# Performance work log

Hardware: AMD Instinct MI355X
Metric: run time of the kernel (lower is better)

The kernel has to match this reference:

```python
import jax, jax.numpy as jnp
import numpy as np

T, D = 4096, 2048
H, DK, DV = 6, 256, 512        # heads, head_k_dim, head_v_dim (expand_v=2)
KD, VD = H * DK, H * DV        # 1536, 3072
KSZ = 4                        # conv_size
GEN = D // 8                   # generator reduction 8 -> 256
EPS = 1e-5                     # norm_eps


def setup_inputs() -> dict:
    key = jax.random.key(0)
    ks = jax.random.split(key, 12)
    std = 0.02
    p = lambda i, shape: jax.random.normal(ks[i], shape, jnp.float32) * std
    rng = np.random.default_rng(0)
    A = rng.uniform(0.0, 16.0, H).astype(np.float32)
    dt = np.exp(rng.uniform(0, 1, H) * (np.log(0.1) - np.log(0.001)) + np.log(0.001)).astype(np.float32)
    dt = np.clip(dt, 1e-4, None)
    inv_dt = (dt + np.log(-np.expm1(-dt))).astype(np.float32)
    return {
        'hidden_states': jax.random.normal(ks[0], (T, D), jnp.float32),
        'Wq': p(1, (D, KD)), 'Wk': p(2, (D, KD)), 'Wv': p(3, (D, VD)),
        'Wb': p(4, (D, H)), 'Wa': p(5, (D, H)), 'Wg': p(6, (D, VD)), 'Wo': p(7, (VD, D)),
        'A_log': jnp.asarray(np.log(A)), 'dt_bias': jnp.asarray(inv_dt),
        'conv_w': p(8, (VD, KSZ)), 'gen_w1': p(9, (D, GEN)), 'gen_w2': p(10, (GEN, KSZ)),
        'norm_w': jnp.ones((DV,), jnp.float32),
    }


def _l2norm(x):
    return x * jax.lax.rsqrt(jnp.sum(x * x, -1, keepdims=True) + 1e-6)


def reference(hidden_states, Wq, Wk, Wv, Wb, Wa, Wg, Wo, A_log, dt_bias, conv_w, gen_w1, gen_w2, norm_w):
    h = hidden_states[None]                             # [1,T,D]
    q = jax.nn.silu(h @ Wq)                             # [1,T,KD]
    k = jax.nn.silu(h @ Wk)
    x = h @ Wv                                          # [1,T,VD]
    # dynamic short convolution: per-token kernel added to static depthwise kernel
    dyn = jax.nn.silu(h @ gen_w1) @ gen_w2              # [1,T,KSZ]
    xpad = jnp.pad(x, ((0, 0), (KSZ - 1, 0), (0, 0)))   # causal padding
    v = jnp.zeros_like(x)
    for j in range(KSZ):
        v = v + (conv_w[None, None, :, j] + dyn[:, :, None, j]) * xpad[:, j:j + x.shape[1], :]
    v = jax.nn.silu(v)

    B = 1
    q = _l2norm(q.reshape(B, -1, H, DK))                # use_qk_l2norm_in_kernel=True
    k = _l2norm(k.reshape(B, -1, H, DK))
    v = v.reshape(B, -1, H, DV)
    beta = jax.nn.sigmoid(h @ Wb)                       # [1,T,H]
    g = -jnp.exp(A_log) * jax.nn.softplus(h @ Wa + dt_bias)  # [1,T,H] decay log-gates
    scale = DK ** -0.5

    def step(S, inp):                                   # gated delta rule recurrence
        qt, kt, vt, gt, bt = inp
        S = S * jnp.exp(gt)[..., None, None]            # [B,H,DK,DV]
        dv = (vt - jnp.einsum('bhk,bhkv->bhv', kt, S)) * bt[..., None]
        S = S + kt[..., :, None] * dv[..., None, :]
        ot = jnp.einsum('bhk,bhkv->bhv', qt, S) * scale
        return S, ot

    S0 = jnp.zeros((B, H, DK, DV), jnp.float32)
    tm = lambda a: jnp.moveaxis(a, 1, 0)                # time-major for scan
    _, o = jax.lax.scan(step, S0, (tm(q), tm(k), tm(v), tm(g), tm(beta)))
    o = jnp.moveaxis(o, 0, 1)                           # [1,T,H,DV]

    gate = (h @ Wg).reshape(B, -1, H, DV)
    rms = jax.lax.rsqrt(jnp.mean(o * o, -1, keepdims=True) + EPS)
    o = o * rms * norm_w * jax.nn.silu(gate)            # gated RMSNorm
    o = o.reshape(B, -1, VD) @ Wo                       # [1,T,D]
    return o[0]
```

## Files before the change

### kernel.cpp

```cpp
#include <hip/hip_runtime.h>
#include <hip/hip_bf16.h>
#include <math.h>

#define T_LEN 4096
#define DIM   2048
#define NH    6
#define DK    256
#define DVh   512
#define KD    1536
#define VD    3072
#define CK    64
#define NCHK  (T_LEN / CK)

typedef __attribute__((ext_vector_type(8))) short bf16x8;
typedef __attribute__((ext_vector_type(4))) float f32x4;

__device__ __forceinline__ float silu_f(float v){ return v / (1.f + __expf(-v)); }

__device__ __forceinline__ unsigned short f2bf(float f) {
  unsigned int u = __float_as_uint(f);
  unsigned int r = u + 0x7FFFu + ((u >> 16) & 1u);
  return (unsigned short)(r >> 16);
}
__device__ __forceinline__ float bf2f(unsigned short s) {
  return __uint_as_float(((unsigned int)s) << 16);
}

__device__ __forceinline__ void bar_lds() {
  __builtin_amdgcn_sched_barrier(0);
  asm volatile("s_waitcnt lgkmcnt(0)" ::: "memory");
  __builtin_amdgcn_s_barrier();
  __builtin_amdgcn_sched_barrier(0);
}

__global__ __launch_bounds__(256) void cast_bf16(
    const float* __restrict__ in, unsigned short* __restrict__ out)
{
  int i = blockIdx.x * 256 + threadIdx.x;
  float4 v4 = ((const float4*)in)[i];
  ushort4 o4;
  o4.x = f2bf(v4.x); o4.y = f2bf(v4.y); o4.z = f2bf(v4.z); o4.w = f2bf(v4.w);
  ((ushort4*)out)[i] = o4;
}

__global__ __launch_bounds__(256) void tcast(
// ... 58 lines not shown
#pragma unroll
    for (int i = 0; i < 4; ++i)
#pragma unroll
      for (int j = 0; j < 4; ++j)
        acc[i][j] = __builtin_amdgcn_mfma_f32_16x16x32_bf16(af[i], bfr[j], acc[i][j], 0, 0, 0);
    __syncthreads();
  }

  if (act == 2) {
    unsigned short* C = (unsigned short*)Cout;
#pragma unroll
    for (int i = 0; i < 4; ++i) {
      int rbase = bm + wm + i * 16 + kq * 4;
#pragma unroll
      for (int r = 0; r < 4; ++r) {
        size_t rowoff = (size_t)(rbase + r) * N + bn + wn + fr;
#pragma unroll
        for (int j = 0; j < 4; ++j) C[rowoff + j * 16] = f2bf(acc[i][j][r]);
      }
    }
  } else {
    float* C = (float*)Cout;
#pragma unroll
    for (int i = 0; i < 4; ++i) {
      int rbase = bm + wm + i * 16 + kq * 4;
#pragma unroll
      for (int r = 0; r < 4; ++r) {
        size_t rowoff = (size_t)(rbase + r) * N + bn + wn + fr;
#pragma unroll
        for (int j = 0; j < 4; ++j) {
          float v = acc[i][j][r];
          if (act == 1) v = silu_f(v);
          C[rowoff + j * 16] = v;
        }
      }
    }
  }
}

__global__ __launch_bounds__(256) void proj_dyn(
    const float* __restrict__ tg, const float* __restrict__ w2, float* __restrict__ dyn)
{
  int t = blockIdx.x, tid = threadIdx.x;
  float g = tg[(size_t)t * 256 + tid];
  float p[4];
#pragma unroll
  for (int j = 0; j < 4; ++j) p[j] = g * w2[tid * 4 + j];
#pragma unroll
  for (int j = 0; j < 4; ++j)
    for (int m = 32; m >= 1; m >>= 1) p[j] += __shfl_xor(p[j], m);
  __shared__ float red[4][4];
  if ((tid & 63) == 0) {
    int w = tid >> 6;
#pragma unroll
    for (int j = 0; j < 4; ++j) red[w][j] = p[j];
  }
  __syncthreads();
  if (tid < 4) dyn[(size_t)t * 4 + tid] = red[0][tid] + red[1][tid] + red[2][tid] + red[3][tid];
}

__global__ __launch_bounds__(256) void proj_bg(
    const float* __restrict__ h, const float* __restrict__ Wb, const float* __restrict__ Wa,
    const float* __restrict__ A_log, const float* __restrict__ dt_bias,
    float* __restrict__ beta, float* __restrict__ gout)
{
  int t = blockIdx.x, tid = threadIdx.x;
// ... 14 lines not shown
  __shared__ float rb[4][6], ra[4][6];
  if ((tid & 63) == 0) {
    int w = tid >> 6;
#pragma unroll
    for (int j = 0; j < 6; ++j) { rb[w][j] = pb[j]; ra[w][j] = pa[j]; }
  }
  __syncthreads();
  if (tid < 6) {
    int j = tid;
    float sb = rb[0][j] + rb[1][j] + rb[2][j] + rb[3][j];
    float sa = ra[0][j] + ra[1][j] + ra[2][j] + ra[3][j];
    beta[(size_t)t * 6 + j] = 1.f / (1.f + expf(-sb));
    float z = sa + dt_bias[j];
    float sp = (z > 20.f) ? z : log1pf(expf(z));
    gout[(size_t)t * 6 + j] = -expf(A_log[j]) * sp;
  }
}

__global__ __launch_bounds__(256) void conv_kernel(
    const float* __restrict__ x, const float* __restrict__ dyn,
    const float* __restrict__ cw, float* __restrict__ v)
{
  int c = blockIdx.x * 256 + threadIdx.x;
  int t = blockIdx.y;
  float4 w4 = ((const float4*)cw)[c];
  float d0 = dyn[t * 4 + 0], d1 = dyn[t * 4 + 1], d2 = dyn[t * 4 + 2], d3 = dyn[t * 4 + 3];
  float acc = (w4.w + d3) * x[(size_t)t * VD + c];
  if (t >= 1) acc += (w4.z + d2) * x[(size_t)(t - 1) * VD + c];
  if (t >= 2) acc += (w4.y + d1) * x[(size_t)(t - 2) * VD + c];
  if (t >= 3) acc += (w4.x + d0) * x[(size_t)(t - 3) * VD + c];
  v[(size_t)t * VD + c] = silu_f(acc);
}

__global__ __launch_bounds__(64) void l2norm_qk(
    float* __restrict__ q, float* __restrict__ k)
{
  size_t base = (size_t)blockIdx.x * 256;
  int tid = threadIdx.x;
  float4 qv = ((float4*)(q + base))[tid];
  float4 kv = ((float4*)(k + base))[tid];
  float sq = qv.x*qv.x + qv.y*qv.y + qv.z*qv.z + qv.w*qv.w;
  float sk = kv.x*kv.x + kv.y*kv.y + kv.z*kv.z + kv.w*kv.w;
  for (int m = 32; m >= 1; m >>= 1) { sq += __shfl_xor(sq, m); sk += __shfl_xor(sk, m); }
  float rq = rsqrtf(sq + 1e-6f) * 0.0625f;
  float rk = rsqrtf(sk + 1e-6f);
  qv.x *= rq; qv.y *= rq; qv.z *= rq; qv.w *= rq;
  kv.x *= rk; kv.y *= rk; kv.z *= rk; kv.w *= rk;
  ((float4*)(q + base))[tid] = qv;
  ((float4*)(k + base))[tid] = kv;
}

__global__ __launch_bounds__(64) void cumsum_g(
    const float* __restrict__ g, float* __restrict__ c, float* __restrict__ gammas)
{
  int ch = blockIdx.x, h = blockIdx.y;
  int t0 = ch * CK;
  int lane = threadIdx.x;
  float cum = g[(size_t)(t0 + lane) * 6 + h];
  for (int off = 1; off < 64; off <<= 1) {
    float n = __shfl_up(cum, off);
    if (lane >= off) cum += n;
  }
  c[(size_t)h * T_LEN + t0 + lane] = cum;
  if (lane == 63) gammas[h * NCHK + ch] = __expf(cum);
}

__global__ __launch_bounds__(384) void scale_kq(
    const float* __restrict__ q, const float* __restrict__ k, const float* __restrict__ c,
    unsigned short* __restrict__ Qb, unsigned short* __restrict__ Kb)
{
  int t = blockIdx.x;
  int tid = threadIdx.x;
  int h = tid >> 6;
  float w1 = __expf(c[(size_t)h * T_LEN + t]);
  size_t off = (size_t)t * KD + tid * 4;
  float4 qv = *(const float4*)(q + off);
  float4 kv = *(const float4*)(k + off);
  ushort4 qo, ko;
  qo.x = f2bf(w1 * qv.x); qo.y = f2bf(w1 * qv.y); qo.z = f2bf(w1 * qv.z); qo.w = f2bf(w1 * qv.w);
  ko.x = f2bf(w1 * kv.x); ko.y = f2bf(w1 * kv.y); ko.z = f2bf(w1 * kv.z); ko.w = f2bf(w1 * kv.w);
  *(ushort4*)(Qb + off) = qo;
  *(ushort4*)(Kb + off) = ko;
}

__global__ __launch_bounds__(256) void make_khT(
    const float* __restrict__ k, const float* __restrict__ c,
    unsigned short* __restrict__ KhT)
{
  int ch = blockIdx.x, h = blockIdx.y;
  int t0 = ch * CK;
  int tt = threadIdx.x & 63, ks = threadIdx.x >> 6;
  float cend = c[(size_t)h * T_LEN + t0 + 63];
  float w2 = __expf(cend - c[(size_t)h * T_LEN + t0 + tt]);
  size_t obase = ((size_t)(h * NCHK + ch)) * DK * CK;
#pragma unroll 8
  for (int kb2 = 0; kb2 < 64; ++kb2) {
    int kk = ks * 64 + kb2;
    float kv = k[(size_t)(t0 + tt) * KD + h * 256 + kk];
    KhT[obase + (size_t)kk * CK + tt] = f2bf(w2 * kv);
  }
}

__global__ __launch_bounds__(256) void chunk_lp(
    const float* __restrict__ q, const float* __restrict__ k,
    const float* __restrict__ c, const float* __restrict__ beta,
    float* __restrict__ Lg, unsigned short* __restrict__ Pm)
{
  const int ch = blockIdx.x, h = blockIdx.y;
  const int t0 = ch * CK;
  const int tid = threadIdx.x;
// ... 16 lines not shown
  if (tid < 64) {
    cs[tid] = c[(size_t)h * T_LEN + t0 + tid];
    bs[tid] = beta[(size_t)(t0 + tid) * 6 + h];
  }
  __syncthreads();

  f32x4 akk[4], aqk[4];
#pragma unroll
  for (int j = 0; j < 4; ++j) { akk[j] = (f32x4){0,0,0,0}; aqk[j] = (f32x4){0,0,0,0}; }
#pragma unroll
  for (int kt = 0; kt < 8; ++kt) {
    bf16x8 ak = *(const bf16x8*)&kb[16 * w + fr][kt * 32 + kq * 8];
    bf16x8 aq = *(const bf16x8*)&qb[16 * w + fr][kt * 32 + kq * 8];
#pragma unroll
    for (int j = 0; j < 4; ++j) {
      bf16x8 b = *(const bf16x8*)&kb[j * 16 + fr][kt * 32 + kq * 8];
      akk[j] = __builtin_amdgcn_mfma_f32_16x16x32_bf16(ak, b, akk[j], 0, 0, 0);
      aqk[j] = __builtin_amdgcn_mfma_f32_16x16x32_bf16(aq, b, aqk[j], 0, 0, 0);
    }
  }
  size_t base = ((size_t)(h * NCHK + ch)) * CK * CK;
#pragma unroll
  for (int j = 0; j < 4; ++j) {
#pragma unroll
    for (int r = 0; r < 4; ++r) {
      int t = 16 * w + kq * 4 + r, col = j * 16 + fr;
      float e = __expf(fminf(cs[t] - cs[col], 0.f));
      Lg[base + t * 64 + col] = (col < t) ? bs[t] * e * akk[j][r] : 0.f;
      Pm[base + t * 64 + col] = f2bf((col <= t) ? e * aqk[j][r] : 0.f);
    }
  }
}

__global__ __launch_bounds__(64) void tri_inv(
    const float* __restrict__ Lg, const float* __restrict__ beta,
    unsigned short* __restrict__ Tm)
{
  const int ch = blockIdx.x, h = blockIdx.y;
  const size_t base = ((size_t)(h * NCHK + ch)) * CK * CK;
  const int j = threadIdx.x;
  __shared__ float Ll[64][65];
  __shared__ float Tl[64][65];
  for (int t = 0; t < 64; ++t) Ll[t][j] = Lg[base + t * 64 + j];
  __syncthreads();
  for (int t = 0; t < 64; ++t) {
    float s;
    if (j > t) s = 0.f;
    else if (j == t) s = 1.f;
    else {
      s = 0.f;
      for (int m = j; m < t; ++m) s -= Ll[t][m] * Tl[m][j];
    }
    Tl[t][j] = s;
  }
  float bj = beta[(size_t)(ch * 64 + j) * 6 + h];
  for (int t = 0; t < 64; ++t) Tm[base + t * 64 + j] = f2bf(Tl[t][j] * bj);
}

__global__ __launch_bounds__(512, 2) void scan_chunk(
    const unsigned short* __restrict__ Kb,
    const unsigned short* __restrict__ Qb,
    const unsigned short* __restrict__ KhT,
    const unsigned short* __restrict__ Tm,
    const unsigned short* __restrict__ Pm,
    const float* __restrict__ gammas,
    float* __restrict__ VO)
{
  const int h = blockIdx.y, sl = blockIdx.x;
  const int tid = threadIdx.x;
  const int w = tid >> 6, lane = tid & 63;
  const int tw = w & 3, kg = w >> 2;
  const int fr = lane & 15, kq = lane >> 4;

  __shared__ unsigned short S0h[16][264];
  __shared__ unsigned short S0l[16][264];
  __shared__ unsigned short XT[16][72];
  __shared__ unsigned short DVT[16][72];
  __shared__ float PY[2][4][16][20];
  __shared__ float PO[2][4][16][20];

  f32x4 st[2];
  st[0] = (f32x4){0.f, 0.f, 0.f, 0.f};
  st[1] = (f32x4){0.f, 0.f, 0.f, 0.f};

  const int colg = h * DVh + sl * 16 + fr;
  const size_t hc0 = (size_t)h * NCHK;

  {
    int zr = tid >> 5;
    int zc = (tid & 31) * 8;
    ushort4 z; z.x = 0; z.y = 0; z.z = 0; z.w = 0;
    *(ushort4*)&S0h[zr][zc]     = z;
    *(ushort4*)&S0h[zr][zc + 4] = z;
    *(ushort4*)&S0l[zr][zc]     = z;
    *(ushort4*)&S0l[zr][zc + 4] = z;
  }

  bf16x8 kfA[4], kfB[4], qfA[4], qfB[4];
  float vlA[4], vlB[4];

#define PREF(KF, QF, VL, chn) do { \
    const unsigned short* kr_ = Kb + (size_t)((chn) * CK + 16 * tw + fr) * KD + h * 256 + kg * 128 + kq * 8; \
    const unsigned short* qr_ = Qb + (size_t)((chn) * CK + 16 * tw + fr) * KD + h * 256 + kg * 128 + kq * 8; \
    _Pragma("unroll") \
    for (int kt = 0; kt < 4; ++kt) { \
      KF[kt] = *(const bf16x8*)(kr_ + kt * 32); \
      QF[kt] = *(const bf16x8*)(qr_ + kt * 32); } \
    if (kg == 0) { \
      _Pragma("unroll") \
      for (int r = 0; r < 4; ++r) VL[r] = VO[(size_t)((chn) * CK + 16 * tw + kq * 4 + r) * VD + colg]; } \
  } while (0)

#define BODY(chx, KF, QF, VL, KFN, QFN, VLN) do { \
    const int ch_ = (chx); \
    const int t0_ = ch_ * CK; \
    const size_t cb_ = hc0 + ch_; \
     \
    bf16x8 tpf[2]; \
    { const unsigned short* b_ = (kg == 0 ? Tm : Pm) + (cb_ * CK + 16 * tw + fr) * CK + kq * 8; \
      tpf[0] = *(const bf16x8*)(b_); tpf[1] = *(const bf16x8*)(b_ + 32); } \
    bf16x8 hfr[2][2]; \
    _Pragma("unroll") \
    for (int i = 0; i < 2; ++i) { \
      const unsigned short* hr_ = KhT + (cb_ * DK + 32 * w + 16 * i + fr) * CK + kq * 8; \
      hfr[i][0] = *(const bf16x8*)(hr_); hfr[i][1] = *(const bf16x8*)(hr_ + 32); } \
    const float gam_ = gammas[cb_]; \
    { const int chn_ = (ch_ + 1 < NCHK) ? ch_ + 1 : ch_; PREF(KFN, QFN, VLN, chn_); } \
     \
    f32x4 yt, ot; \
    { f32x4 yh = (f32x4){0.f,0.f,0.f,0.f}, yl = yh, oh = yh, ol = yh; \
      __builtin_amdgcn_s_setprio(1); \
      _Pragma("unroll") \
      for (int kt = 0; kt < 4; ++kt) { \
        const int ka_ = (kg * 4 + kt) * 32 + kq * 8; \
        bf16x8 bh_ = *(const bf16x8*)&S0h[fr][ka_]; \
        bf16x8 bl_ = *(const bf16x8*)&S0l[fr][ka_]; \
        yh = __builtin_amdgcn_mfma_f32_16x16x32_bf16(KF[kt], bh_, yh, 0, 0, 0); \
        yl = __builtin_amdgcn_mfma_f32_16x16x32_bf16(KF[kt], bl_, yl, 0, 0, 0); \
        oh = __builtin_amdgcn_mfma_f32_16x16x32_bf16(QF[kt], bh_, oh, 0, 0, 0); \
        ol = __builtin_amdgcn_mfma_f32_16x16x32_bf16(QF[kt], bl_, ol, 0, 0, 0); } \
      __builtin_amdgcn_s_setprio(0); \
      yt = yh + yl; ot = oh + ol; } \
    *(f32x4*)&PY[kg][tw][fr][kq * 4] = yt; \
    *(f32x4*)&PO[kg][tw][fr][kq * 4] = ot; \
    bar_lds();    \
    if (kg == 0) { \
      f32x4 yo = *(const f32x4*)&PY[1][tw][fr][kq * 4]; \
      ushort4 x4; \
      x4.x = f2bf(VL[0] - (yt[0] + yo[0])); \
      x4.y = f2bf(VL[1] - (yt[1] + yo[1])); \
      x4.z = f2bf(VL[2] - (yt[2] + yo[2])); \
      x4.w = f2bf(VL[3] - (yt[3] + yo[3])); \
      *(ushort4*)&XT[fr][16 * tw + kq * 4] = x4; \
    } else { \
      f32x4 oo = *(const f32x4*)&PO[0][tw][fr][kq * 4]; \
      ot[0] += oo[0]; ot[1] += oo[1]; ot[2] += oo[2]; ot[3] += oo[3]; } \
    bar_lds();    \
     \
    if (kg == 0) { \
      f32x4 d = (f32x4){0.f,0.f,0.f,0.f}; \
      bf16x8 b0_ = *(const bf16x8*)&XT[fr][kq * 8]; \
      bf16x8 b1_ = *(const bf16x8*)&XT[fr][32 + kq * 8]; \
      d = __builtin_amdgcn_mfma_f32_16x16x32_bf16(tpf[0], b0_, d, 0, 0, 0); \
      d = __builtin_amdgcn_mfma_f32_16x16x32_bf16(tpf[1], b1_, d, 0, 0, 0); \
      ushort4 d4; \
      d4.x = f2bf(d[0]); d4.y = f2bf(d[1]); d4.z = f2bf(d[2]); d4.w = f2bf(d[3]); \
      *(ushort4*)&DVT[fr][16 * tw + kq * 4] = d4; } \
    bar_lds();    \
     \
    { bf16x8 dv0_ = *(const bf16x8*)&DVT[fr][kq * 8]; \
      bf16x8 dv1_ = *(const bf16x8*)&DVT[fr][32 + kq * 8]; \
      if (kg == 1) { \
        f32x4 op = (f32x4){0.f,0.f,0.f,0.f}; \
        op = __builtin_amdgcn_mfma_f32_16x16x32_bf16(tpf[0], dv0_, op, 0, 0, 0); \
        op = __builtin_amdgcn_mfma_f32_16x16x32_bf16(tpf[1], dv1_, op, 0, 0, 0); \
        _Pragma("unroll") \
        for (int r = 0; r < 4; ++r) \
          VO[(size_t)(t0_ + 16 * tw + kq * 4 + r) * VD + colg] = ot[r] + op[r]; } \
      __builtin_amdgcn_s_setprio(1); \
      _Pragma("unroll") \
      for (int i = 0; i < 2; ++i) { \
        st[i][0] *= gam_; st[i][1] *= gam_; st[i][2] *= gam_; st[i][3] *= gam_; \
        st[i] = __builtin_amdgcn_mfma_f32_16x16x32_bf16(hfr[i][0], dv0_, st[i], 0, 0, 0); \
        st[i] = __builtin_amdgcn_mfma_f32_16x16x32_bf16(hfr[i][1], dv1_, st[i], 0, 0, 0); \
        ushort4 hi4, lo4; \
        { float s0 = st[i][0], s1 = st[i][1], s2 = st[i][2], s3 = st[i][3]; \
          hi4.x = f2bf(s0); lo4.x = f2bf(s0 - bf2f(hi4.x)); \
          hi4.y = f2bf(s1); lo4.y = f2bf(s1 - bf2f(hi4.y)); \
          hi4.z = f2bf(s2); lo4.z = f2bf(s2 - bf2f(hi4.z)); \
          hi4.w = f2bf(s3); lo4.w = f2bf(s3 - bf2f(hi4.w)); } \
        *(ushort4*)&S0h[fr][32 * w + 16 * i + kq * 4] = hi4; \
        *(ushort4*)&S0l[fr][32 * w + 16 * i + kq * 4] = lo4; } \
      __builtin_amdgcn_s_setprio(0); } \
    bar_lds();    \
  } while (0)

  PREF(kfA, qfA, vlA, 0);
  __syncthreads();
  for (int ch = 0; ch < NCHK; ch += 2) {
    BODY(ch,     kfA, qfA, vlA, kfB, qfB, vlB);
    BODY(ch + 1, kfB, qfB, vlB, kfA, qfA, vlA);
  }
#undef BODY
#undef PREF
}

__global__ __launch_bounds__(256) void norm_gate(
    const float* __restrict__ o, const unsigned short* __restrict__ gate,
    const float* __restrict__ nw, unsigned short* __restrict__ out)
{
  int th = blockIdx.x, tid = threadIdx.x;
  size_t base = (size_t)th * DVh;
  float x0 = o[base + tid], x1 = o[base + 256 + tid];
  float ss = x0 * x0 + x1 * x1;
  for (int m = 32; m >= 1; m >>= 1) ss += __shfl_xor(ss, m);
  __shared__ float red[4];
  if ((tid & 63) == 0) red[tid >> 6] = ss;
  __syncthreads();
  float rms = rsqrtf((red[0] + red[1] + red[2] + red[3]) * (1.f / 512.f) + 1e-5f);
  float g0 = bf2f(gate[base + tid]), g1 = bf2f(gate[base + 256 + tid]);
  out[base + tid]       = f2bf(x0 * rms * nw[tid]       * silu_f(g0));
  out[base + 256 + tid] = f2bf(x1 * rms * nw[tid + 256] * silu_f(g1));
}

extern "C" void kernel_launch(void* const* d_in, const int* in_sizes, int n_in,
                              void* d_out, int out_size, void* d_ws, size_t ws_size,
                              hipStream_t stream)
{
  const float* h       = (const float*)d_in[0];
  const float* Wq      = (const float*)d_in[1];
  const float* Wk      = (const float*)d_in[2];
  const float* Wv      = (const float*)d_in[3];
  const float* Wb      = (const float*)d_in[4];
  const float* Wa      = (const float*)d_in[5];
  const float* Wg      = (const float*)d_in[6];
  const float* Wo      = (const float*)d_in[7];
  const float* A_log   = (const float*)d_in[8];
  const float* dt_bias = (const float*)d_in[9];
  const float* conv_w  = (const float*)d_in[10];
  const float* gen_w1  = (const float*)d_in[11];
  const float* gen_w2  = (const float*)d_in[12];
  const float* norm_w  = (const float*)d_in[13];
  float* out = (float*)d_out;

  const size_t TK = (size_t)T_LEN * KD, TV = (size_t)T_LEN * VD, TD = (size_t)T_LEN * DIM;

  float* ws   = (float*)d_ws;
  float* q    = ws;
  float* k    = q    + TK;
  float* x    = k    + TK;
  float* v    = x    + TV;
  float* tg   = v    + TV;
  float* dyn  = tg   + (size_t)T_LEN * 256;
  float* beta = dyn  + (size_t)T_LEN * 4;
  float* g    = beta + (size_t)T_LEN * 6;
  float* c    = g    + (size_t)T_LEN * 6;
  float* gam  = c    + (size_t)NH * T_LEN;
  float* fend = gam  + 512;
  unsigned short* bh      = (unsigned short*)fend;
  unsigned short* wT      = bh      + TD;
  unsigned short* gate_bf = wT      + (size_t)DIM * VD;
  unsigned short* go_bf   = gate_bf + TV;
  unsigned short* Kb_s  = bh;
  unsigned short* Qb_s  = (unsigned short*)x;
  unsigned short* KhT_s = Qb_s + TK;
  unsigned short* Tm_s  = KhT_s + TK;
  unsigned short* Pm_s  = Tm_s + (size_t)NH * NCHK * CK * CK;
  float* Lg = (float*)go_bf;

  dim3 blk(256);
  cast_bf16<<<(TD / 4) / 256, blk, 0, stream>>>(h, bh);
  tcast<<<dim3(KD / 32, DIM / 32), blk, 0, stream>>>(Wq, wT, DIM, KD);
  gemm_bt_bf16<<<dim3(KD / 128, T_LEN / 128), blk, 0, stream>>>(bh, wT, q, T_LEN, KD, DIM, 1);
  tcast<<<dim3(KD / 32, DIM / 32), blk, 0, stream>>>(Wk, wT, DIM, KD);
  gemm_bt_bf16<<<dim3(KD / 128, T_LEN / 128), blk, 0, stream>>>(bh, wT, k, T_LEN, KD, DIM, 1);
  tcast<<<dim3(VD / 32, DIM / 32), blk, 0, stream>>>(Wv, wT, DIM, VD);
  gemm_bt_bf16<<<dim3(VD / 128, T_LEN / 128), blk, 0, stream>>>(bh, wT, x, T_LEN, VD, DIM, 0);
  tcast<<<dim3(VD / 32, DIM / 32), blk, 0, stream>>>(Wg, wT, DIM, VD);
  gemm_bt_bf16<<<dim3(VD / 128, T_LEN / 128), blk, 0, stream>>>(bh, wT, gate_bf, T_LEN, VD, DIM, 2);
  tcast<<<dim3(256 / 32, DIM / 32), blk, 0, stream>>>(gen_w1, wT, DIM, 256);
  gemm_bt_bf16<<<dim3(256 / 128, T_LEN / 128), blk, 0, stream>>>(bh, wT, tg, T_LEN, 256, DIM, 1);

  proj_dyn<<<T_LEN, blk, 0, stream>>>(tg, gen_w2, dyn);
  proj_bg<<<T_LEN, blk, 0, stream>>>(h, Wb, Wa, A_log, dt_bias, beta, g);
  conv_kernel<<<dim3(VD / 256, T_LEN), blk, 0, stream>>>(x, dyn, conv_w, v);
  l2norm_qk<<<T_LEN * NH, 64, 0, stream>>>(q, k);

  cumsum_g<<<dim3(NCHK, NH), 64, 0, stream>>>(g, c, gam);
  scale_kq<<<T_LEN, 384, 0, stream>>>(q, k, c, Qb_s, Kb_s);
  make_khT<<<dim3(NCHK, NH), blk, 0, stream>>>(k, c, KhT_s);
  chunk_lp<<<dim3(NCHK, NH), blk, 0, stream>>>(q, k, c, beta, Lg, Pm_s);
  tri_inv<<<dim3(NCHK, NH), 64, 0, stream>>>(Lg, beta, Tm_s);

  scan_chunk<<<dim3(DVh / 16, NH), 512, 0, stream>>>(Kb_s, Qb_s, KhT_s, Tm_s, Pm_s, gam, v);

  norm_gate<<<T_LEN * NH, blk, 0, stream>>>(v, gate_bf, norm_w, go_bf);
  tcast<<<dim3(DIM / 32, VD / 32), blk, 0, stream>>>(Wo, wT, VD, DIM);
  gemm_bt_bf16<<<dim3(DIM / 128, T_LEN / 128), blk, 0, stream>>>(go_bf, wT, out, T_LEN, DIM, VD, 0);
}
```

Measured before the change: 1.035 ms.

## Process chunk pairs in scan with precomputed cross-chunk interaction matrices

Adds a cross_lp kernel that precomputes, for each pair of consecutive chunks, the decayed K2·K1ᵀ and Q2·K1ᵀ interaction matrices. The sequential scan now advances two chunks per iteration. The second chunk's state projections reuse the first chunk's pre-update state, corrected through these matrices. This halves the number of serial state reads and LDS round-trips along the critical path, and removes the cross-warp partial-sum reduction. The cost is an extra kernel, more register pressure (launch bounds drop to one block per SM), and additional bf16 rounding in the correction terms.

```diff
diff --git a/kernel.cpp b/kernel.cpp
--- a/kernel.cpp
+++ b/kernel.cpp
@@ -11,6 +11,7 @@
 #define VD    3072
 #define CK    64
 #define NCHK  (T_LEN / CK)
+#define NPAIR (NCHK / 2)
 
 typedef __attribute__((ext_vector_type(8))) short bf16x8;
 typedef __attribute__((ext_vector_type(4))) float f32x4;
@@ -341,6 +342,63 @@
   }
 }
 
+__global__ __launch_bounds__(256) void cross_lp(
+    const unsigned short* __restrict__ Kb, const unsigned short* __restrict__ Qb,
+    const float* __restrict__ k, const float* __restrict__ c,
+    unsigned short* __restrict__ W21, unsigned short* __restrict__ U21)
+{
+  const int p = blockIdx.x, h = blockIdx.y;
+  const int t01 = p * 128, t02 = t01 + 64;
+  const int tid = threadIdx.x;
+  const int w = tid >> 6, lane = tid & 63, fr = lane & 15, kq = lane >> 4;
+  __shared__ float wg[64];
+  if (tid < 64) {
+    float cend = c[(size_t)h * T_LEN + t01 + 63];
+    wg[tid] = __expf(cend - c[(size_t)h * T_LEN + t01 + tid]);
+  }
+  __syncthreads();
+  bf16x8 kfr[8], qfr[8];
+  {
+    const unsigned short* kr = Kb + (size_t)(t02 + 16 * w + fr) * KD + h * 256 + kq * 8;
+    const unsigned short* qr = Qb + (size_t)(t02 + 16 * w + fr) * KD + h * 256 + kq * 8;
+#pragma unroll
+    for (int kt = 0; kt < 8; ++kt) {
+      kfr[kt] = *(const bf16x8*)(kr + kt * 32);
+      qfr[kt] = *(const bf16x8*)(qr + kt * 32);
+    }
+  }
+  f32x4 aw[4], au[4];
+#pragma unroll
+  for (int j = 0; j < 4; ++j) { aw[j] = (f32x4){0,0,0,0}; au[j] = (f32x4){0,0,0,0}; }
+#pragma unroll
+  for (int kt = 0; kt < 8; ++kt) {
+#pragma unroll
+    for (int j2 = 0; j2 < 4; ++j2) {
+      int t1 = j2 * 16 + fr;
+      float wt = wg[t1];
+      const float* kp = k + (size_t)(t01 + t1) * KD + h * 256 + kt * 32 + kq * 8;
+      float4 a0 = *(const float4*)(kp);
+      float4 a1 = *(const float4*)(kp + 4);
+      bf16x8 b;
+      b[0] = (short)f2bf(wt * a0.x); b[1] = (short)f2bf(wt * a0.y);
+      b[2] = (short)f2bf(wt * a0.z); b[3] = (short)f2bf(wt * a0.w);
+      b[4] = (short)f2bf(wt * a1.x); b[5] = (short)f2bf(wt * a1.y);
+      b[6] = (short)f2bf(wt * a1.z); b[7] = (short)f2bf(wt * a1.w);
+      aw[j2] = __builtin_amdgcn_mfma_f32_16x16x32_bf16(kfr[kt], b, aw[j2], 0, 0, 0);
+      au[j2] = __builtin_amdgcn_mfma_f32_16x16x32_bf16(qfr[kt], b, au[j2], 0, 0, 0);
+    }
+  }
+  size_t pb = ((size_t)h * NPAIR + p) * 4096;
+#pragma unroll
+  for (int j2 = 0; j2 < 4; ++j2)
+#pragma unroll
+    for (int r = 0; r < 4; ++r) {
+      int t2 = 16 * w + kq * 4 + r, t1 = j2 * 16 + fr;
+      W21[pb + (size_t)t2 * 64 + t1] = f2bf(aw[j2][r]);
+      U21[pb + (size_t)t2 * 64 + t1] = f2bf(au[j2][r]);
+    }
+}
+
 __global__ __launch_bounds__(64) void tri_inv(
     const float* __restrict__ Lg, const float* __restrict__ beta,
     unsigned short* __restrict__ Tm)
@@ -366,27 +424,27 @@
   for (int t = 0; t < 64; ++t) Tm[base + t * 64 + j] = f2bf(Tl[t][j] * bj);
 }
 
-__global__ __launch_bounds__(512, 2) void scan_chunk(
+__global__ __launch_bounds__(512, 1) void scan_pair(
     const unsigned short* __restrict__ Kb,
     const unsigned short* __restrict__ Qb,
     const unsigned short* __restrict__ KhT,
     const unsigned short* __restrict__ Tm,
     const unsigned short* __restrict__ Pm,
+    const unsigned short* __restrict__ W21,
+    const unsigned short* __restrict__ U21,
     const float* __restrict__ gammas,
     float* __restrict__ VO)
 {
   const int h = blockIdx.y, sl = blockIdx.x;
   const int tid = threadIdx.x;
   const int w = tid >> 6, lane = tid & 63;
-  const int tw = w & 3, kg = w >> 2;
+  const int hf = w >> 2, tw = w & 3;
   const int fr = lane & 15, kq = lane >> 4;
 
   __shared__ unsigned short S0h[16][264];
   __shared__ unsigned short S0l[16][264];
-  __shared__ unsigned short XT[16][72];
-  __shared__ unsigned short DVT[16][72];
-  __shared__ float PY[2][4][16][20];
-  __shared__ float PO[2][4][16][20];
+  __shared__ unsigned short XT[2][16][72];
+  __shared__ unsigned short DVT[2][16][72];
 
   f32x4 st[2];
   st[0] = (f32x4){0.f, 0.f, 0.f, 0.f};
@@ -394,10 +452,11 @@
 
   const int colg = h * DVh + sl * 16 + fr;
   const size_t hc0 = (size_t)h * NCHK;
+  const int trow = 16 * tw + kq * 4;
+  const int frow = 16 * tw + fr;
 
   {
-    int zr = tid >> 5;
-    int zc = (tid & 31) * 8;
+    int zr = tid >> 5, zc = (tid & 31) * 8;
     ushort4 z; z.x = 0; z.y = 0; z.z = 0; z.w = 0;
     *(ushort4*)&S0h[zr][zc]     = z;
     *(ushort4*)&S0h[zr][zc + 4] = z;
@@ -405,110 +464,145 @@
     *(ushort4*)&S0l[zr][zc + 4] = z;
   }
 
-  bf16x8 kfA[4], kfB[4], qfA[4], qfB[4];
+  bf16x8 kfA[8], kfB[8];
   float vlA[4], vlB[4];
 
-#define PREF(KF, QF, VL, chn) do { \
-    const unsigned short* kr_ = Kb + (size_t)((chn) * CK + 16 * tw + fr) * KD + h * 256 + kg * 128 + kq * 8; \
-    const unsigned short* qr_ = Qb + (size_t)((chn) * CK + 16 * tw + fr) * KD + h * 256 + kg * 128 + kq * 8; \
+#define PREF(KF, VL, pp) do { \
+    const unsigned short* kr_ = Kb + (size_t)((pp) * 128 + hf * 64 + frow) * KD + h * 256 + kq * 8; \
     _Pragma("unroll") \
-    for (int kt = 0; kt < 4; ++kt) { \
-      KF[kt] = *(const bf16x8*)(kr_ + kt * 32); \
-      QF[kt] = *(const bf16x8*)(qr_ + kt * 32); } \
-    if (kg == 0) { \
+    for (int kt = 0; kt < 8; ++kt) KF[kt] = *(const bf16x8*)(kr_ + kt * 32); \
+    _Pragma("unroll") \
+    for (int r = 0; r < 4; ++r) \
+      VL[r] = VO[(size_t)((pp) * 128 + hf * 64 + trow + r) * VD + colg]; \
+  } while (0)
+
+#define BODY(pp, KF, VL, KFN, VLN) do { \
+    const int p_ = (pp); \
+    const int t0_ = p_ * 128; \
+    const size_t cb1_ = hc0 + 2 * p_, cb2_ = cb1_ + 1; \
+    const size_t cbx_ = hf ? cb2_ : cb1_; \
+    bf16x8 qf[8]; \
+    { const unsigned short* qr_ = Qb + (size_t)(t0_ + hf * 64 + frow) * KD + h * 256 + kq * 8; \
       _Pragma("unroll") \
-      for (int r = 0; r < 4; ++r) VL[r] = VO[(size_t)((chn) * CK + 16 * tw + kq * 4 + r) * VD + colg]; } \
-  } while (0)
-
-#define BODY(chx, KF, QF, VL, KFN, QFN, VLN) do { \
-    const int ch_ = (chx); \
-    const int t0_ = ch_ * CK; \
-    const size_t cb_ = hc0 + ch_; \
-     \
-    bf16x8 tpf[2]; \
-    { const unsigned short* b_ = (kg == 0 ? Tm : Pm) + (cb_ * CK + 16 * tw + fr) * CK + kq * 8; \
-      tpf[0] = *(const bf16x8*)(b_); tpf[1] = *(const bf16x8*)(b_ + 32); } \
-    bf16x8 hfr[2][2]; \
+      for (int kt = 0; kt < 8; ++kt) qf[kt] = *(const bf16x8*)(qr_ + kt * 32); } \
+    bf16x8 tpa[2], ppa[2]; \
+    { const unsigned short* tr_ = Tm + (cbx_ * CK + frow) * CK + kq * 8; \
+      tpa[0] = *(const bf16x8*)(tr_); tpa[1] = *(const bf16x8*)(tr_ + 32); \
+      const unsigned short* pr_ = Pm + (cbx_ * CK + frow) * CK + kq * 8; \
+      ppa[0] = *(const bf16x8*)(pr_); ppa[1] = *(const bf16x8*)(pr_ + 32); } \
+    bf16x8 wuf[4]; \
+    if (hf) { \
+      const size_t pb_ = ((size_t)h * NPAIR + p_) * 4096; \
+      const unsigned short* wr_ = W21 + pb_ + (size_t)frow * 64 + kq * 8; \
+      wuf[0] = *(const bf16x8*)(wr_); wuf[1] = *(const bf16x8*)(wr_ + 32); \
+      const unsigned short* ur_ = U21 + pb_ + (size_t)frow * 64 + kq * 8; \
+      wuf[2] = *(const bf16x8*)(ur_); wuf[3] = *(const bf16x8*)(ur_ + 32); } \
+    bf16x8 kh1[2][2], kh2[2][2]; \
     _Pragma("unroll") \
     for (int i = 0; i < 2; ++i) { \
-      const unsigned short* hr_ = KhT + (cb_ * DK + 32 * w + 16 * i + fr) * CK + kq * 8; \
-      hfr[i][0] = *(const bf16x8*)(hr_); hfr[i][1] = *(const bf16x8*)(hr_ + 32); } \
-    const float gam_ = gammas[cb_]; \
-    { const int chn_ = (ch_ + 1 < NCHK) ? ch_ + 1 : ch_; PREF(KFN, QFN, VLN, chn_); } \
+      const unsigned short* h1_ = KhT + (cb1_ * DK + 32 * w + 16 * i + fr) * CK + kq * 8; \
+      kh1[i][0] = *(const bf16x8*)(h1_); kh1[i][1] = *(const bf16x8*)(h1_ + 32); \
+      const unsigned short* h2_ = KhT + (cb2_ * DK + 32 * w + 16 * i + fr) * CK + kq * 8; \
+      kh2[i][0] = *(const bf16x8*)(h2_); kh2[i][1] = *(const bf16x8*)(h2_ + 32); } \
+    const float g1_ = gammas[cb1_], g2_ = gammas[cb2_]; \
+    { const int pn_ = (p_ + 1 < NPAIR) ? p_ + 1 : p_; PREF(KFN, VLN, pn_); } \
      \
     f32x4 yt, ot; \
     { f32x4 yh = (f32x4){0.f,0.f,0.f,0.f}, yl = yh, oh = yh, ol = yh; \
-      __builtin_amdgcn_s_setprio(1); \
       _Pragma("unroll") \
-      for (int kt = 0; kt < 4; ++kt) { \
-        const int ka_ = (kg * 4 + kt) * 32 + kq * 8; \
-        bf16x8 bh_ = *(const bf16x8*)&S0h[fr][ka_]; \
-        bf16x8 bl_ = *(const bf16x8*)&S0l[fr][ka_]; \
+      for (int kt = 0; kt < 8; ++kt) { \
+        bf16x8 bh_ = *(const bf16x8*)&S0h[fr][kt * 32 + kq * 8]; \
+        bf16x8 bl_ = *(const bf16x8*)&S0l[fr][kt * 32 + kq * 8]; \
         yh = __builtin_amdgcn_mfma_f32_16x16x32_bf16(KF[kt], bh_, yh, 0, 0, 0); \
         yl = __builtin_amdgcn_mfma_f32_16x16x32_bf16(KF[kt], bl_, yl, 0, 0, 0); \
-        oh = __builtin_amdgcn_mfma_f32_16x16x32_bf16(QF[kt], bh_, oh, 0, 0, 0); \
-        ol = __builtin_amdgcn_mfma_f32_16x16x32_bf16(QF[kt], bl_, ol, 0, 0, 0); } \
-      __builtin_amdgcn_s_setprio(0); \
+        oh = __builtin_amdgcn_mfma_f32_16x16x32_bf16(qf[kt], bh_, oh, 0, 0, 0); \
+        ol = __builtin_amdgcn_mfma_f32_16x16x32_bf16(qf[kt], bl_, ol, 0, 0, 0); } \
       yt = yh + yl; ot = oh + ol; } \
-    *(f32x4*)&PY[kg][tw][fr][kq * 4] = yt; \
-    *(f32x4*)&PO[kg][tw][fr][kq * 4] = ot; \
+    if (hf == 0) { \
+      ushort4 x4; \
+      x4.x = f2bf(VL[0] - yt[0]); x4.y = f2bf(VL[1] - yt[1]); \
+      x4.z = f2bf(VL[2] - yt[2]); x4.w = f2bf(VL[3] - yt[3]); \
+      *(ushort4*)&XT[0][fr][trow] = x4; } \
     bar_lds();    \
-    if (kg == 0) { \
-      f32x4 yo = *(const f32x4*)&PY[1][tw][fr][kq * 4]; \
-      ushort4 x4; \
-      x4.x = f2bf(VL[0] - (yt[0] + yo[0])); \
-      x4.y = f2bf(VL[1] - (yt[1] + yo[1])); \
-      x4.z = f2bf(VL[2] - (yt[2] + yo[2])); \
-      x4.w = f2bf(VL[3] - (yt[3] + yo[3])); \
-      *(ushort4*)&XT[fr][16 * tw + kq * 4] = x4; \
-    } else { \
-      f32x4 oo = *(const f32x4*)&PO[0][tw][fr][kq * 4]; \
-      ot[0] += oo[0]; ot[1] += oo[1]; ot[2] += oo[2]; ot[3] += oo[3]; } \
-    bar_lds();    \
-     \
-    if (kg == 0) { \
+    if (hf == 0) { \
       f32x4 d = (f32x4){0.f,0.f,0.f,0.f}; \
-      bf16x8 b0_ = *(const bf16x8*)&XT[fr][kq * 8]; \
-      bf16x8 b1_ = *(const bf16x8*)&XT[fr][32 + kq * 8]; \
-      d = __builtin_amdgcn_mfma_f32_16x16x32_bf16(tpf[0], b0_, d, 0, 0, 0); \
-      d = __builtin_amdgcn_mfma_f32_16x16x32_bf16(tpf[1], b1_, d, 0, 0, 0); \
+      bf16x8 b0_ = *(const bf16x8*)&XT[0][fr][kq * 8]; \
+      bf16x8 b1_ = *(const bf16x8*)&XT[0][fr][32 + kq * 8]; \
+      d = __builtin_amdgcn_mfma_f32_16x16x32_bf16(tpa[0], b0_, d, 0, 0, 0); \
+      d = __builtin_amdgcn_mfma_f32_16x16x32_bf16(tpa[1], b1_, d, 0, 0, 0); \
       ushort4 d4; \
       d4.x = f2bf(d[0]); d4.y = f2bf(d[1]); d4.z = f2bf(d[2]); d4.w = f2bf(d[3]); \
-      *(ushort4*)&DVT[fr][16 * tw + kq * 4] = d4; } \
+      *(ushort4*)&DVT[0][fr][trow] = d4; } \
     bar_lds();    \
+    bf16x8 dv10 = *(const bf16x8*)&DVT[0][fr][kq * 8]; \
+    bf16x8 dv11 = *(const bf16x8*)&DVT[0][fr][32 + kq * 8]; \
+    if (hf == 0) { \
+      f32x4 op = (f32x4){0.f,0.f,0.f,0.f}; \
+      op = __builtin_amdgcn_mfma_f32_16x16x32_bf16(ppa[0], dv10, op, 0, 0, 0); \
+      op = __builtin_amdgcn_mfma_f32_16x16x32_bf16(ppa[1], dv11, op, 0, 0, 0); \
+      _Pragma("unroll") \
+      for (int r = 0; r < 4; ++r) \
+        VO[(size_t)(t0_ + trow + r) * VD + colg] = ot[r] + op[r]; \
+    } else { \
+      f32x4 xw = (f32x4){0.f,0.f,0.f,0.f}; \
+      xw = __builtin_amdgcn_mfma_f32_16x16x32_bf16(wuf[0], dv10, xw, 0, 0, 0); \
+      xw = __builtin_amdgcn_mfma_f32_16x16x32_bf16(wuf[1], dv11, xw, 0, 0, 0); \
+      ushort4 x4; \
+      x4.x = f2bf(VL[0] - g1_ * yt[0] - xw[0]); \
+      x4.y = f2bf(VL[1] - g1_ * yt[1] - xw[1]); \
+      x4.z = f2bf(VL[2] - g1_ * yt[2] - xw[2]); \
+      x4.w = f2bf(VL[3] - g1_ * yt[3] - xw[3]); \
+      *(ushort4*)&XT[1][fr][trow] = x4; } \
      \
-    { bf16x8 dv0_ = *(const bf16x8*)&DVT[fr][kq * 8]; \
-      bf16x8 dv1_ = *(const bf16x8*)&DVT[fr][32 + kq * 8]; \
-      if (kg == 1) { \
-        f32x4 op = (f32x4){0.f,0.f,0.f,0.f}; \
-        op = __builtin_amdgcn_mfma_f32_16x16x32_bf16(tpf[0], dv0_, op, 0, 0, 0); \
-        op = __builtin_amdgcn_mfma_f32_16x16x32_bf16(tpf[1], dv1_, op, 0, 0, 0); \
-        _Pragma("unroll") \
-        for (int r = 0; r < 4; ++r) \
-          VO[(size_t)(t0_ + 16 * tw + kq * 4 + r) * VD + colg] = ot[r] + op[r]; } \
-      __builtin_amdgcn_s_setprio(1); \
+    _Pragma("unroll") \
+    for (int i = 0; i < 2; ++i) { \
+      st[i][0] *= g1_; st[i][1] *= g1_; st[i][2] *= g1_; st[i][3] *= g1_; \
+      st[i] = __builtin_amdgcn_mfma_f32_16x16x32_bf16(kh1[i][0], dv10, st[i], 0, 0, 0); \
+      st[i] = __builtin_amdgcn_mfma_f32_16x16x32_bf16(kh1[i][1], dv11, st[i], 0, 0, 0); } \
+    bar_lds();    \
+    if (hf) { \
+      f32x4 d = (f32x4){0.f,0.f,0.f,0.f}; \
+      bf16x8 b0_ = *(const bf16x8*)&XT[1][fr][kq * 8]; \
+      bf16x8 b1_ = *(const bf16x8*)&XT[1][fr][32 + kq * 8]; \
+      d = __builtin_amdgcn_mfma_f32_16x16x32_bf16(tpa[0], b0_, d, 0, 0, 0); \
+      d = __builtin_amdgcn_mfma_f32_16x16x32_bf16(tpa[1], b1_, d, 0, 0, 0); \
+      ushort4 d4; \
+      d4.x = f2bf(d[0]); d4.y = f2bf(d[1]); d4.z = f2bf(d[2]); d4.w = f2bf(d[3]); \
+      *(ushort4*)&DVT[1][fr][trow] = d4; } \
+    bar_lds();    \
+    bf16x8 dv20 = *(const bf16x8*)&DVT[1][fr][kq * 8]; \
+    bf16x8 dv21 = *(const bf16x8*)&DVT[1][fr][32 + kq * 8]; \
+    if (hf) { \
+      f32x4 op = (f32x4){0.f,0.f,0.f,0.f}; \
+      op = __builtin_amdgcn_mfma_f32_16x16x32_bf16(wuf[2], dv10, op, 0, 0, 0); \
+      op = __builtin_amdgcn_mfma_f32_16x16x32_bf16(wuf[3], dv11, op, 0, 0, 0); \
+      op = __builtin_amdgcn_mfma_f32_16x16x32_bf16(ppa[0], dv20, op, 0, 0, 0); \
+      op = __builtin_amdgcn_mfma_f32_16x16x32_bf16(ppa[1], dv21, op, 0, 0, 0); \
       _Pragma("unroll") \
-      for (int i = 0; i < 2; ++i) { \
-        st[i][0] *= gam_; st[i][1] *= gam_; st[i][2] *= gam_; st[i][3] *= gam_; \
-        st[i] = __builtin_amdgcn_mfma_f32_16x16x32_bf16(hfr[i][0], dv0_, st[i], 0, 0, 0); \
-        st[i] = __builtin_amdgcn_mfma_f32_16x16x32_bf16(hfr[i][1], dv1_, st[i], 0, 0, 0); \
-        ushort4 hi4, lo4; \
-        { float s0 = st[i][0], s1 = st[i][1], s2 = st[i][2], s3 = st[i][3]; \
-          hi4.x = f2bf(s0); lo4.x = f2bf(s0 - bf2f(hi4.x)); \
-          hi4.y = f2bf(s1); lo4.y = f2bf(s1 - bf2f(hi4.y)); \
-          hi4.z = f2bf(s2); lo4.z = f2bf(s2 - bf2f(hi4.z)); \
-          hi4.w = f2bf(s3); lo4.w = f2bf(s3 - bf2f(hi4.w)); } \
-        *(ushort4*)&S0h[fr][32 * w + 16 * i + kq * 4] = hi4; \
-        *(ushort4*)&S0l[fr][32 * w + 16 * i + kq * 4] = lo4; } \
-      __builtin_amdgcn_s_setprio(0); } \
+      for (int r = 0; r < 4; ++r) \
+        VO[(size_t)(t0_ + 64 + trow + r) * VD + colg] = g1_ * ot[r] + op[r]; } \
+     \
+    _Pragma("unroll") \
+    for (int i = 0; i < 2; ++i) { \
+      st[i][0] *= g2_; st[i][1] *= g2_; st[i][2] *= g2_; st[i][3] *= g2_; \
+      st[i] = __builtin_amdgcn_mfma_f32_16x16x32_bf16(kh2[i][0], dv20, st[i], 0, 0, 0); \
+      st[i] = __builtin_amdgcn_mfma_f32_16x16x32_bf16(kh2[i][1], dv21, st[i], 0, 0, 0); \
+      ushort4 hi4, lo4; \
+      { float s0 = st[i][0], s1 = st[i][1], s2 = st[i][2], s3 = st[i][3]; \
+        hi4.x = f2bf(s0); lo4.x = f2bf(s0 - bf2f(hi4.x)); \
+        hi4.y = f2bf(s1); lo4.y = f2bf(s1 - bf2f(hi4.y)); \
+        hi4.z = f2bf(s2); lo4.z = f2bf(s2 - bf2f(hi4.z)); \
+        hi4.w = f2bf(s3); lo4.w = f2bf(s3 - bf2f(hi4.w)); } \
+      *(ushort4*)&S0h[fr][32 * w + 16 * i + kq * 4] = hi4; \
+      *(ushort4*)&S0l[fr][32 * w + 16 * i + kq * 4] = lo4; } \
     bar_lds();    \
   } while (0)
 
-  PREF(kfA, qfA, vlA, 0);
+  PREF(kfA, vlA, 0);
   __syncthreads();
-  for (int ch = 0; ch < NCHK; ch += 2) {
-    BODY(ch,     kfA, qfA, vlA, kfB, qfB, vlB);
-    BODY(ch + 1, kfB, qfB, vlB, kfA, qfA, vlA);
+  for (int p = 0; p < NPAIR; p += 2) {
+    BODY(p,     kfA, vlA, kfB, vlB);
+    BODY(p + 1, kfB, vlB, kfA, vlA);
   }
 #undef BODY
 #undef PREF
@@ -575,6 +669,8 @@
   unsigned short* KhT_s = Qb_s + TK;
   unsigned short* Tm_s  = KhT_s + TK;
   unsigned short* Pm_s  = Tm_s + (size_t)NH * NCHK * CK * CK;
+  unsigned short* W21_s = Pm_s + (size_t)NH * NCHK * CK * CK;
+  unsigned short* U21_s = W21_s + (size_t)NH * NPAIR * 64 * 64;
   float* Lg = (float*)go_bf;
 
   dim3 blk(256);
@@ -597,11 +693,13 @@
 
   cumsum_g<<<dim3(NCHK, NH), 64, 0, stream>>>(g, c, gam);
   scale_kq<<<T_LEN, 384, 0, stream>>>(q, k, c, Qb_s, Kb_s);
+  cross_lp<<<dim3(NPAIR, NH), blk, 0, stream>>>(Kb_s, Qb_s, k, c, W21_s, U21_s);
   make_khT<<<dim3(NCHK, NH), blk, 0, stream>>>(k, c, KhT_s);
   chunk_lp<<<dim3(NCHK, NH), blk, 0, stream>>>(q, k, c, beta, Lg, Pm_s);
   tri_inv<<<dim3(NCHK, NH), 64, 0, stream>>>(Lg, beta, Tm_s);
 
-  scan_chunk<<<dim3(DVh / 16, NH), 512, 0, stream>>>(Kb_s, Qb_s, KhT_s, Tm_s, Pm_s, gam, v);
+  scan_pair<<<dim3(DVh / 16, NH), 512, 0, stream>>>(
+      Kb_s, Qb_s, KhT_s, Tm_s, Pm_s, W21_s, U21_s, gam, v);
 
   norm_gate<<<T_LEN * NH, blk, 0, stream>>>(v, gate_bf, norm_w, go_bf);
   tcast<<<dim3(DIM / 32, VD / 32), blk, 0, stream>>>(Wo, wT, VD, DIM);
```

Result: slower. 1.065 ms (+2.9%).

## Batch input projections into one concatenated GEMM and fuse l2norm with scaling

Applied to the files above, without the earlier changes.

The five input-projection GEMMs (q, k, v, gate, generator) become one launch. Their transposed bf16 weights are concatenated into a single buffer placed in the not-yet-used v region, and each 128-column tile picks its output buffer and epilogue by column range. This cuts launch count, fills the GPU better than the small 256-column generator GEMM did alone, and reads the shared A operand within one kernel. Separately, the l2norm and the decay-scaling/bf16 cast kernels are merged so q and k are read once fewer times. The cost is reusing the v buffer for weights, which is only safe because v is written after the fused GEMM.

```diff
diff --git a/kernel.cpp b/kernel.cpp
--- a/kernel.cpp
+++ b/kernel.cpp
@@ -11,6 +11,7 @@
 #define VD    3072
 #define CK    64
 #define NCHK  (T_LEN / CK)
+#define NFUSE 9472
 
 typedef __attribute__((ext_vector_type(8))) short bf16x8;
 typedef __attribute__((ext_vector_type(4))) float f32x4;
@@ -135,6 +136,96 @@
           float v = acc[i][j][r];
           if (act == 1) v = silu_f(v);
           C[rowoff + j * 16] = v;
+        }
+      }
+    }
+  }
+}
+
+__global__ __launch_bounds__(256) void gemm_fused(
+    const unsigned short* __restrict__ A, const unsigned short* __restrict__ BT,
+    float* __restrict__ Cq, float* __restrict__ Ck, float* __restrict__ Cx,
+    unsigned short* __restrict__ Cg, float* __restrict__ Ct)
+{
+  __shared__ unsigned short As[128 * 32];
+  __shared__ unsigned short Bs[128 * 32];
+  const int tid = threadIdx.x;
+  const int bm = blockIdx.y * 128, bn = blockIdx.x * 128;
+  const int lane = tid & 63, wave = tid >> 6;
+  const int wm = (wave >> 1) * 64, wn = (wave & 1) * 64;
+  const int fr = lane & 15, kq = lane >> 4;
+  const int K = DIM;
+
+  f32x4 acc[4][4];
+#pragma unroll
+  for (int i = 0; i < 4; ++i)
+#pragma unroll
+    for (int j = 0; j < 4; ++j) acc[i][j] = (f32x4){0.f, 0.f, 0.f, 0.f};
+
+  const int r0 = tid >> 2, c0 = (tid & 3) * 8;
+  const int r1 = r0 + 64;
+
+  for (int k0 = 0; k0 < K; k0 += 32) {
+    __builtin_amdgcn_global_load_lds(
+        (const __attribute__((address_space(1))) unsigned int*)(A + (size_t)(bm + r0) * K + k0 + c0),
+        (__attribute__((address_space(3))) unsigned int*)(As + r0 * 32 + c0), 16, 0, 0);
+    __builtin_amdgcn_global_load_lds(
+        (const __attribute__((address_space(1))) unsigned int*)(A + (size_t)(bm + r1) * K + k0 + c0),
+        (__attribute__((address_space(3))) unsigned int*)(As + r1 * 32 + c0), 16, 0, 0);
+    __builtin_amdgcn_global_load_lds(
+        (const __attribute__((address_space(1))) unsigned int*)(BT + (size_t)(bn + r0) * K + k0 + c0),
+        (__attribute__((address_space(3))) unsigned int*)(Bs + r0 * 32 + c0), 16, 0, 0);
+    __builtin_amdgcn_global_load_lds(
+        (const __attribute__((address_space(1))) unsigned int*)(BT + (size_t)(bn + r1) * K + k0 + c0),
+        (__attribute__((address_space(3))) unsigned int*)(Bs + r1 * 32 + c0), 16, 0, 0);
+    __syncthreads();
+
+    bf16x8 af[4], bfr[4];
+#pragma unroll
+    for (int i = 0; i < 4; ++i)
+      af[i] = *(const bf16x8*)(As + (wm + i * 16 + fr) * 32 + kq * 8);
+#pragma unroll
+    for (int j = 0; j < 4; ++j)
+      bfr[j] = *(const bf16x8*)(Bs + (wn + j * 16 + fr) * 32 + kq * 8);
+#pragma unroll
+    for (int i = 0; i < 4; ++i)
+#pragma unroll
+      for (int j = 0; j < 4; ++j)
+        acc[i][j] = __builtin_amdgcn_mfma_f32_16x16x32_bf16(af[i], bfr[j], acc[i][j], 0, 0, 0);
+    __syncthreads();
+  }
+
+  float* Fd = nullptr; unsigned short* Bd = nullptr;
+  int strideN, cb, mode;
+  if (bn < 1536)      { Fd = Cq; strideN = 1536; cb = bn;        mode = 1; }
+  else if (bn < 3072) { Fd = Ck; strideN = 1536; cb = bn - 1536; mode = 1; }
+  else if (bn < 6144) { Fd = Cx; strideN = 3072; cb = bn - 3072; mode = 0; }
+  else if (bn < 9216) { Bd = Cg; strideN = 3072; cb = bn - 6144; mode = 2; }
+  else                { Fd = Ct; strideN = 256;  cb = bn - 9216; mode = 1; }
+
+  if (mode == 2) {
+#pragma unroll
+    for (int i = 0; i < 4; ++i) {
+      int rbase = bm + wm + i * 16 + kq * 4;
+#pragma unroll
+      for (int r = 0; r < 4; ++r) {
+        size_t rowoff = (size_t)(rbase + r) * strideN + cb + wn + fr;
+#pragma unroll
+        for (int j = 0; j < 4; ++j) Bd[rowoff + j * 16] = f2bf(acc[i][j][r]);
+      }
+    }
+  } else {
+#pragma unroll
+    for (int i = 0; i < 4; ++i) {
+      int rbase = bm + wm + i * 16 + kq * 4;
+#pragma unroll
+      for (int r = 0; r < 4; ++r) {
+        size_t rowoff = (size_t)(rbase + r) * strideN + cb + wn + fr;
+#pragma unroll
+        for (int j = 0; j < 4; ++j) {
+          float v = acc[i][j][r];
+          if (mode == 1) v = silu_f(v);
+          Fd[rowoff + j * 16] = v;
         }
       }
     }
@@ -215,13 +306,30 @@
   v[(size_t)t * VD + c] = silu_f(acc);
 }
 
-__global__ __launch_bounds__(64) void l2norm_qk(
-    float* __restrict__ q, float* __restrict__ k)
-{
-  size_t base = (size_t)blockIdx.x * 256;
-  int tid = threadIdx.x;
-  float4 qv = ((float4*)(q + base))[tid];
-  float4 kv = ((float4*)(k + base))[tid];
+__global__ __launch_bounds__(64) void cumsum_g(
+    const float* __restrict__ g, float* __restrict__ c, float* __restrict__ gammas)
+{
+  int ch = blockIdx.x, h = blockIdx.y;
+  int t0 = ch * CK;
+  int lane = threadIdx.x;
+  float cum = g[(size_t)(t0 + lane) * 6 + h];
+  for (int off = 1; off < 64; off <<= 1) {
+    float n = __shfl_up(cum, off);
+    if (lane >= off) cum += n;
+  }
+  c[(size_t)h * T_LEN + t0 + lane] = cum;
+  if (lane == 63) gammas[h * NCHK + ch] = __expf(cum);
+}
+
+__global__ __launch_bounds__(384) void l2scale(
+    float* __restrict__ q, float* __restrict__ k, const float* __restrict__ c,
+    unsigned short* __restrict__ Qb, unsigned short* __restrict__ Kb)
+{
+  int t = blockIdx.x;
+  int h = threadIdx.x >> 6, lane = threadIdx.x & 63;
+  size_t off = (size_t)t * KD + h * 256 + lane * 4;
+  float4 qv = *(const float4*)(q + off);
+  float4 kv = *(const float4*)(k + off);
   float sq = qv.x*qv.x + qv.y*qv.y + qv.z*qv.z + qv.w*qv.w;
   float sk = kv.x*kv.x + kv.y*kv.y + kv.z*kv.z + kv.w*kv.w;
   for (int m = 32; m >= 1; m >>= 1) { sq += __shfl_xor(sq, m); sk += __shfl_xor(sk, m); }
@@ -229,36 +337,9 @@
   float rk = rsqrtf(sk + 1e-6f);
   qv.x *= rq; qv.y *= rq; qv.z *= rq; qv.w *= rq;
   kv.x *= rk; kv.y *= rk; kv.z *= rk; kv.w *= rk;
-  ((float4*)(q + base))[tid] = qv;
-  ((float4*)(k + base))[tid] = kv;
-}
-
-__global__ __launch_bounds__(64) void cumsum_g(
-    const float* __restrict__ g, float* __restrict__ c, float* __restrict__ gammas)
-{
-  int ch = blockIdx.x, h = blockIdx.y;
-  int t0 = ch * CK;
-  int lane = threadIdx.x;
-  float cum = g[(size_t)(t0 + lane) * 6 + h];
-  for (int off = 1; off < 64; off <<= 1) {
-    float n = __shfl_up(cum, off);
-    if (lane >= off) cum += n;
-  }
-  c[(size_t)h * T_LEN + t0 + lane] = cum;
-  if (lane == 63) gammas[h * NCHK + ch] = __expf(cum);
-}
-
-__global__ __launch_bounds__(384) void scale_kq(
-    const float* __restrict__ q, const float* __restrict__ k, const float* __restrict__ c,
-    unsigned short* __restrict__ Qb, unsigned short* __restrict__ Kb)
-{
-  int t = blockIdx.x;
-  int tid = threadIdx.x;
-  int h = tid >> 6;
+  *(float4*)(q + off) = qv;
+  *(float4*)(k + off) = kv;
   float w1 = __expf(c[(size_t)h * T_LEN + t]);
-  size_t off = (size_t)t * KD + tid * 4;
-  float4 qv = *(const float4*)(q + off);
-  float4 kv = *(const float4*)(k + off);
   ushort4 qo, ko;
   qo.x = f2bf(w1 * qv.x); qo.y = f2bf(w1 * qv.y); qo.z = f2bf(w1 * qv.z); qo.w = f2bf(w1 * qv.w);
   ko.x = f2bf(w1 * kv.x); ko.y = f2bf(w1 * kv.y); ko.z = f2bf(w1 * kv.z); ko.w = f2bf(w1 * kv.w);
@@ -576,27 +657,24 @@
   unsigned short* Tm_s  = KhT_s + TK;
   unsigned short* Pm_s  = Tm_s + (size_t)NH * NCHK * CK * CK;
   float* Lg = (float*)go_bf;
+  unsigned short* wTall = (unsigned short*)v;
 
   dim3 blk(256);
   cast_bf16<<<(TD / 4) / 256, blk, 0, stream>>>(h, bh);
-  tcast<<<dim3(KD / 32, DIM / 32), blk, 0, stream>>>(Wq, wT, DIM, KD);
-  gemm_bt_bf16<<<dim3(KD / 128, T_LEN / 128), blk, 0, stream>>>(bh, wT, q, T_LEN, KD, DIM, 1);
-  tcast<<<dim3(KD / 32, DIM / 32), blk, 0, stream>>>(Wk, wT, DIM, KD);
-  gemm_bt_bf16<<<dim3(KD / 128, T_LEN / 128), blk, 0, stream>>>(bh, wT, k, T_LEN, KD, DIM, 1);
-  tcast<<<dim3(VD / 32, DIM / 32), blk, 0, stream>>>(Wv, wT, DIM, VD);
-  gemm_bt_bf16<<<dim3(VD / 128, T_LEN / 128), blk, 0, stream>>>(bh, wT, x, T_LEN, VD, DIM, 0);
-  tcast<<<dim3(VD / 32, DIM / 32), blk, 0, stream>>>(Wg, wT, DIM, VD);
-  gemm_bt_bf16<<<dim3(VD / 128, T_LEN / 128), blk, 0, stream>>>(bh, wT, gate_bf, T_LEN, VD, DIM, 2);
-  tcast<<<dim3(256 / 32, DIM / 32), blk, 0, stream>>>(gen_w1, wT, DIM, 256);
-  gemm_bt_bf16<<<dim3(256 / 128, T_LEN / 128), blk, 0, stream>>>(bh, wT, tg, T_LEN, 256, DIM, 1);
-
+  tcast<<<dim3(KD / 32, DIM / 32), blk, 0, stream>>>(Wq, wTall + (size_t)0 * DIM, DIM, KD);
+  tcast<<<dim3(KD / 32, DIM / 32), blk, 0, stream>>>(Wk, wTall + (size_t)1536 * DIM, DIM, KD);
+  tcast<<<dim3(VD / 32, DIM / 32), blk, 0, stream>>>(Wv, wTall + (size_t)3072 * DIM, DIM, VD);
+  tcast<<<dim3(VD / 32, DIM / 32), blk, 0, stream>>>(Wg, wTall + (size_t)6144 * DIM, DIM, VD);
+  tcast<<<dim3(256 / 32, DIM / 32), blk, 0, stream>>>(gen_w1, wTall + (size_t)9216 * DIM, DIM, 256);
+  gemm_fused<<<dim3(NFUSE / 128, T_LEN / 128), blk, 0, stream>>>(
+      bh, wTall, q, k, x, gate_bf, tg);
+
+  proj_bg<<<T_LEN, blk, 0, stream>>>(h, Wb, Wa, A_log, dt_bias, beta, g);
+  cumsum_g<<<dim3(NCHK, NH), 64, 0, stream>>>(g, c, gam);
   proj_dyn<<<T_LEN, blk, 0, stream>>>(tg, gen_w2, dyn);
-  proj_bg<<<T_LEN, blk, 0, stream>>>(h, Wb, Wa, A_log, dt_bias, beta, g);
   conv_kernel<<<dim3(VD / 256, T_LEN), blk, 0, stream>>>(x, dyn, conv_w, v);
-  l2norm_qk<<<T_LEN * NH, 64, 0, stream>>>(q, k);
-
-  cumsum_g<<<dim3(NCHK, NH), 64, 0, stream>>>(g, c, gam);
-  scale_kq<<<T_LEN, 384, 0, stream>>>(q, k, c, Qb_s, Kb_s);
+  l2scale<<<T_LEN, 384, 0, stream>>>(q, k, c, Qb_s, Kb_s);
+
   make_khT<<<dim3(NCHK, NH), blk, 0, stream>>>(k, c, KhT_s);
   chunk_lp<<<dim3(NCHK, NH), blk, 0, stream>>>(q, k, c, beta, Lg, Pm_s);
   tri_inv<<<dim3(NCHK, NH), 64, 0, stream>>>(Lg, beta, Tm_s);
```

New measurement: 981.8 us. 5.1% less time.
